# Kernel optimization log

Hardware: AMD Instinct MI355X
Metric: run time of the kernel (lower is better)

The kernel has to match this reference:

```python
import jax, jax.numpy as jnp
import numpy as np

B, N, D = 16, 128, 3          # batch, atoms per graph, spatial dims
C, L = 128, 3                 # hidden channels, EGNN layers
NUM_ATOM_TYPE, NUM_AA_TYPE = 54, 20
NUM_AA_MAX, NUM_VALID_SEQ = 30, 26   # num_aa_min=5 -> 30-5+1=26
ENC = NUM_ATOM_TYPE + NUM_AA_MAX + NUM_AA_TYPE + NUM_VALID_SEQ + 1  # 131


def setup_inputs() -> dict:
    key = jax.random.key(0)
    ks = jax.random.split(key, 16)
    f32 = jnp.float32
    def lin(k, fi, fo, scale=1.0):
        return (jax.random.normal(k, (L, fi, fo), f32) * (scale / np.sqrt(fi))).astype(f32)
    return {
        "t": jax.random.uniform(ks[0], (B, 1), f32),
        "x": jax.random.normal(ks[1], (B, N * D), f32),
        "atom_type": jax.random.randint(ks[2], (B, N), 0, NUM_ATOM_TYPE),
        "aa_pos": jax.random.randint(ks[3], (B, N), 0, NUM_AA_MAX),
        "aa_type": jax.random.randint(ks[4], (B, N), 0, NUM_AA_TYPE),
        "seq_len": jax.random.randint(ks[5], (B, 1), 5, 31),
        "node_mask": jnp.ones((B, N), f32),
        "emb_W": (jax.random.normal(ks[6], (ENC, C), f32) / np.sqrt(ENC)).astype(f32),
        "emb_b": jnp.zeros((C,), f32),
        "We1": lin(ks[7], 2 * C + 2, C), "be1": jnp.zeros((L, C), f32),
        "We2": lin(ks[8], C, C),        "be2": jnp.zeros((L, C), f32),
        "Wa": lin(ks[9], C, 1),         "ba": jnp.zeros((L, 1), f32),
        "Wn1": lin(ks[10], 2 * C, C),   "bn1": jnp.zeros((L, C), f32),
        "Wn2": lin(ks[11], C, C),       "bn2": jnp.zeros((L, C), f32),
        "Wc1": lin(ks[12], C, C),       "bc1": jnp.zeros((L, C), f32),
        "Wc2": lin(ks[13], C, 1, scale=0.01),
    }


def _forward(t, x, atom_type, aa_pos, aa_type, seq_len, node_mask,
             emb_W, emb_b, We1, be1, We2, be2, Wa, ba,
             Wn1, bn1, Wn2, bn2, Wc1, bc1, Wc2):
    mask = node_mask.reshape(B * N, 1)
    xf = x.reshape(B * N, D) * mask                       # masked coords

    # time feature: (B,1) -> (B*N,1)
    tt = jnp.repeat(t, N, axis=1).reshape(B * N, 1) * mask

    # one-hot node features (clamp(enc-1, min=0) then one_hot)
    oh_atom = jax.nn.one_hot(jnp.clip(atom_type - 1, 0), NUM_ATOM_TYPE)
    oh_pos = jax.nn.one_hot(jnp.clip(aa_pos - 1, 0), NUM_AA_MAX)
    oh_aa = jax.nn.one_hot(jnp.clip(aa_type - 1, 0), NUM_AA_TYPE)
    se = jnp.clip(seq_len - NUM_AA_MAX + NUM_VALID_SEQ - 1, 0)  # (B,1)
    oh_sl = jax.nn.one_hot(jnp.broadcast_to(se, (B, N)), NUM_VALID_SEQ)
    h = jnp.concatenate([oh_atom, oh_pos, oh_aa, oh_sl], axis=-1)
    h = h.reshape(B * N, -1) * mask
    h = jnp.concatenate([h, tt], axis=-1)                 # (B*N, ENC)

    # fully-connected edges (incl. self-edges, masked out by edge_mask)
    ii = jnp.arange(N)
    base = jnp.arange(B)[:, None, None] * N
    row = jnp.broadcast_to(base + ii[None, :, None], (B, N, N)).reshape(-1)
    col = jnp.broadcast_to(base + ii[None, None, :], (B, N, N)).reshape(-1)
    edge_mask = (node_mask[:, :, None] * node_mask[:, None, :]
                 * (1.0 - jnp.eye(N, dtype=node_mask.dtype))).reshape(-1, 1)

    edge_attr = jnp.sum((xf[row] - xf[col]) ** 2, axis=-1, keepdims=True)

    h = h @ emb_W + emb_b
    xcur = xf
    for l in range(L):
        diff = xcur[row] - xcur[col]                      # (E, 3)
        radial = jnp.sum(diff * diff, axis=-1, keepdims=True)
        m = jnp.concatenate([h[row], h[col], radial, edge_attr], axis=-1)
        m = jax.nn.silu(m @ We1[l] + be1[l])
        m = jax.nn.silu(m @ We2[l] + be2[l])
        m = m * jax.nn.sigmoid(m @ Wa[l] + ba[l])         # attention gate
        m = m * edge_mask
        # equivariant coordinate update
        c = jax.nn.silu(m @ Wc1[l] + bc1[l])
        trans = diff * jnp.tanh(c @ Wc2[l])
        xcur = (xcur + jax.ops.segment_sum(trans, row, num_segments=B * N)) * mask
        # node update (recurrent/residual)
        agg = jax.ops.segment_sum(m, row, num_segments=B * N)
        hn = jax.nn.silu(jnp.concatenate([h, agg], axis=-1) @ Wn1[l] + bn1[l])
        hn = hn @ Wn2[l] + bn2[l]
        h = (h + hn) * mask

    vel = ((xcur - xf) * mask).reshape(B, N, D)
    m3 = node_mask.reshape(B, N, 1)
    cnt = jnp.sum(m3, axis=1, keepdims=True)
    vel = vel - (jnp.sum(vel, axis=1, keepdims=True) / cnt) * m3
    return vel.reshape(B, N * D)


def reference(t, x, atom_type, aa_pos, aa_type, seq_len, node_mask,
              emb_W, emb_b, We1, be1, We2, be2, Wa, ba,
              Wn1, bn1, Wn2, bn2, Wc1, bc1, Wc2):
    return _forward(t, x, atom_type, aa_pos, aa_type, seq_len, node_mask,
                    emb_W, emb_b, We1, be1, We2, be2, Wa, ba,
                    Wn1, bn1, Wn2, bn2, Wc1, bc1, Wc2)
```

## Files before the change

kernel.cpp:

```cpp
#include <hip/hip_runtime.h>
#include <math.h>

#define CC 128

typedef float  f32x4  __attribute__((ext_vector_type(4)));
typedef short  s16x8  __attribute__((ext_vector_type(8)));
typedef __bf16 bf16x8 __attribute__((ext_vector_type(8)));

__device__ __forceinline__ float fsilu(float x) { return x / (1.0f + __expf(-x)); }
__device__ __forceinline__ float fsigm(float x) { return 1.0f / (1.0f + __expf(-x)); }
__device__ __forceinline__ float ftanh_(float x) { return 1.0f - 2.0f / (__expf(2.0f * x) + 1.0f); }

__device__ __forceinline__ void bsplit(float x, short& hi, short& lo) {
    unsigned xu = __float_as_uint(x);
    unsigned hr = (xu + 0x7FFFu + ((xu >> 16) & 1u)) & 0xFFFF0000u;
    float hf = __uint_as_float(hr);
    float r = x - hf;
    unsigned ru = __float_as_uint(r);
    unsigned lr = ru + 0x7FFFu + ((ru >> 16) & 1u);
    hi = (short)(hr >> 16);
    lo = (short)(lr >> 16);
}

__device__ __forceinline__ f32x4 mfma16(s16x8 a, s16x8 b, f32x4 c) {
    return __builtin_amdgcn_mfma_f32_16x16x32_bf16(
        __builtin_bit_cast(bf16x8, a), __builtin_bit_cast(bf16x8, b), c, 0, 0, 0);
}

__global__ __launch_bounds__(128) void egnn_init(
    const float* __restrict__ t, const float* __restrict__ x,
    const int* __restrict__ atomt, const int* __restrict__ aapos,
    const int* __restrict__ aatype, const int* __restrict__ slen,
    const float* __restrict__ nmask, const float* __restrict__ embW,
    const float* __restrict__ embB, float* __restrict__ h,
    float* __restrict__ xf, float* __restrict__ xA)
{
    const int n = blockIdx.x;
    const int c = threadIdx.x;
    const int b = n >> 7;
    const int i = n & 127;
    const float mi = nmask[n];
    int ia = atomt[n] - 1; if (ia < 0) ia = 0;
    int ip = aapos[n] - 1; if (ip < 0) ip = 0;
    int iq = aatype[n] - 1; if (iq < 0) iq = 0;
    int is = slen[b] - 5;  if (is < 0) is = 0;
    const float tt = t[b] * mi;
    float v = mi * (embW[ia * CC + c] + embW[(54 + ip) * CC + c] +
                    embW[(84 + iq) * CC + c] + embW[(104 + is) * CC + c]) +
              tt * embW[130 * CC + c] + embB[c];
    h[(size_t)n * CC + c] = v;
    if (c < 3) {
        float xv = x[b * 384 + i * 3 + c] * mi;
        xf[3 * n + c] = xv;
        xA[3 * n + c] = xv;
    }
}

__global__ __launch_bounds__(128) void egnn_wtprep(
    const float* __restrict__ We2, const float* __restrict__ Wc1,
    short* __restrict__ wt)
{
    const int blk = blockIdx.x;
    const int l = blk >> 5;
    const int mat = (blk >> 4) & 1;
    const int chunk = blk & 15;
    const int k = threadIdx.x;
    const float* W = (mat == 0 ? We2 : Wc1) + (size_t)l * CC * CC;
    short* hi = wt + (size_t)(l * 2 + mat) * 32768;
    short* lo = hi + 16384;
#pragma unroll
    for (int nn = 0; nn < 8; ++nn) {
        const int n = chunk * 8 + nn;
        short h_, l_;
        bsplit(W[k * CC + n], h_, l_);
        hi[n * CC + k] = h_;
        lo[n * CC + k] = l_;
    }
}

__global__ __launch_bounds__(128) void egnn_pq(
    const float* __restrict__ h, const float* __restrict__ We1,
    const float* __restrict__ be1, float* __restrict__ P, float* __restrict__ Q)
{
    __shared__ float hs[2][CC];
    const int c = threadIdx.x;
    const int n0 = blockIdx.x * 2;
    hs[0][c] = h[(size_t)n0 * CC + c];
    hs[1][c] = h[(size_t)(n0 + 1) * CC + c];
    __syncthreads();
    const float bv = be1[c];
    float p0 = bv, p1 = bv, q0 = 0.f, q1 = 0.f;
#pragma unroll 4
    for (int k = 0; k < CC; ++k) {
        const float wr = We1[k * CC + c];
        const float wc = We1[(CC + k) * CC + c];
        p0 = fmaf(hs[0][k], wr, p0); p1 = fmaf(hs[1][k], wr, p1);
        q0 = fmaf(hs[0][k], wc, q0); q1 = fmaf(hs[1][k], wc, q1);
    }
    P[(size_t)n0 * CC + c] = p0; P[(size_t)(n0 + 1) * CC + c] = p1;
    Q[(size_t)n0 * CC + c] = q0; Q[(size_t)(n0 + 1) * CC + c] = q1;
}

__global__ __launch_bounds__(256, 2) void egnn_edge(
    const float* __restrict__ P, const float* __restrict__ Q,
    const float* __restrict__ xcur, const float* __restrict__ xf,
    const float* __restrict__ nmask, const float* __restrict__ We1t,
    const short* __restrict__ w1hiP, const short* __restrict__ w2hiP,
    const float* __restrict__ be2, const float* __restrict__ Wa,
    const float* __restrict__ ba, const float* __restrict__ bc1,
    const float* __restrict__ Wc2,
    float* __restrict__ xnext, float* __restrict__ agg)
{
    extern __shared__ char smraw[];
    short* mhi = (short*)smraw;
    short* mlo = mhi + 16384;
    float* fb    = (float*)(mlo + 16384);
    float* diffs = fb;
    float* rjs   = fb + 384;
    float* eas   = fb + 512;
    float* emks  = fb + 640;
    float* pis   = fb + 768;
    float* wrads = fb + 896;
    float* weas  = fb + 1024;
    float* wass  = fb + 1152;
    float* wc2s  = fb + 1280;
    float* be2s  = fb + 1408;
    float* bc1s  = fb + 1536;
    float* aggp  = fb + 1664;
    float* trp   = fb + 2176;

    const int tid = threadIdx.x;
    const int w  = tid >> 6;
    const int lane = tid & 63;
    const int g  = lane >> 4;
    const int lj = lane & 15;
    const int n = blockIdx.x;
    const int b = n >> 7;
    const int i = n & 127;
    const int nb = b << 7;
    const float mi = nmask[n];

    const short* w1lo = w1hiP + 16384;
    const short* w2lo = w2hiP + 16384;

    if (tid < 128) {
        const int j = tid;
        const float xi0 = xcur[3 * n], xi1 = xcur[3 * n + 1], xi2 = xcur[3 * n + 2];
        const float xj0 = xcur[3 * (nb + j)], xj1 = xcur[3 * (nb + j) + 1], xj2 = xcur[3 * (nb + j) + 2];
        const float d0 = xi0 - xj0, d1 = xi1 - xj1, d2 = xi2 - xj2;
        diffs[3 * j] = d0; diffs[3 * j + 1] = d1; diffs[3 * j + 2] = d2;
        rjs[j] = d0 * d0 + d1 * d1 + d2 * d2;
        const float f0 = xf[3 * n] - xf[3 * (nb + j)];
        const float f1 = xf[3 * n + 1] - xf[3 * (nb + j) + 1];
        const float f2 = xf[3 * n + 2] - xf[3 * (nb + j) + 2];
        eas[j] = f0 * f0 + f1 * f1 + f2 * f2;
        emks[j] = mi * nmask[nb + j] * ((j == i) ? 0.0f : 1.0f);
    } else {
        const int c = tid - 128;
        pis[c]   = P[(size_t)n * CC + c];
        wrads[c] = We1t[c];
        weas[c]  = We1t[CC + c];
        wass[c]  = Wa[c];
        wc2s[c]  = Wc2[c];
        be2s[c]  = be2[c];
        bc1s[c]  = bc1[c];
    }
    __syncthreads();

    s16x8 ahi[2][4], alo[2][4];
#pragma unroll
    for (int mt = 0; mt < 2; ++mt) {
        const int j = (w << 5) + (mt << 4) + lj;
        const float r  = rjs[j];
        const float ea = eas[j];
        const float* Qj = Q + (size_t)(nb + j) * CC;
#pragma unroll
        for (int kt = 0; kt < 4; ++kt) {
            const int c0 = (kt << 5) + (g << 3);
            const float4 q0 = *reinterpret_cast<const float4*>(Qj + c0);
            const float4 q1 = *reinterpret_cast<const float4*>(Qj + c0 + 4);
            const float4 p0 = *reinterpret_cast<const float4*>(pis + c0);
            const float4 p1 = *reinterpret_cast<const float4*>(pis + c0 + 4);
            const float4 r0 = *reinterpret_cast<const float4*>(wrads + c0);
            const float4 r1 = *reinterpret_cast<const float4*>(wrads + c0 + 4);
            const float4 e0 = *reinterpret_cast<const float4*>(weas + c0);
            const float4 e1 = *reinterpret_cast<const float4*>(weas + c0 + 4);
            float vv[8];
            vv[0] = fsilu(p0.x + q0.x + r * r0.x + ea * e0.x);
            vv[1] = fsilu(p0.y + q0.y + r * r0.y + ea * e0.y);
            vv[2] = fsilu(p0.z + q0.z + r * r0.z + ea * e0.z);
            vv[3] = fsilu(p0.w + q0.w + r * r0.w + ea * e0.w);
            vv[4] = fsilu(p1.x + q1.x + r * r1.x + ea * e1.x);
            vv[5] = fsilu(p1.y + q1.y + r * r1.y + ea * e1.y);
            vv[6] = fsilu(p1.z + q1.z + r * r1.z + ea * e1.z);
            vv[7] = fsilu(p1.w + q1.w + r * r1.w + ea * e1.w);
#pragma unroll
            for (int e = 0; e < 8; ++e) {
                short h_, l_;
                bsplit(vv[e], h_, l_);
                ahi[mt][kt][e] = h_;
                alo[mt][kt][e] = l_;
            }
        }
    }

    f32x4 acc[2][8];
#pragma unroll
    for (int mt = 0; mt < 2; ++mt)
#pragma unroll
        for (int nt = 0; nt < 8; ++nt) acc[mt][nt] = (f32x4){0.f, 0.f, 0.f, 0.f};
#pragma unroll
    for (int kt = 0; kt < 4; ++kt) {
#pragma unroll
        for (int nt = 0; nt < 8; ++nt) {
            const int wo = ((nt << 4) + lj) * CC + (kt << 5) + (g << 3);
            const s16x8 bh = *reinterpret_cast<const s16x8*>(w1hiP + wo);
            const s16x8 bl = *reinterpret_cast<const s16x8*>(w1lo + wo);
#pragma unroll
            for (int mt = 0; mt < 2; ++mt) {
                acc[mt][nt] = mfma16(ahi[mt][kt], bh, acc[mt][nt]);
                acc[mt][nt] = mfma16(ahi[mt][kt], bl, acc[mt][nt]);
                acc[mt][nt] = mfma16(alo[mt][kt], bh, acc[mt][nt]);
            }
        }
    }

    float pa[2][4];
#pragma unroll
    for (int mt = 0; mt < 2; ++mt)
#pragma unroll
        for (int r = 0; r < 4; ++r) pa[mt][r] = 0.f;
#pragma unroll
    for (int mt = 0; mt < 2; ++mt)
#pragma unroll
        for (int nt = 0; nt < 8; ++nt) {
            const int c = (nt << 4) + lj;
            const float be = be2s[c], wa = wass[c];
#pragma unroll
            for (int r = 0; r < 4; ++r) {
                const float v = fsilu(acc[mt][nt][r] + be);
                acc[mt][nt][r] = v;
                pa[mt][r] = fmaf(v, wa, pa[mt][r]);
            }
        }
#pragma unroll
    for (int o = 1; o < 16; o <<= 1)
#pragma unroll
        for (int mt = 0; mt < 2; ++mt)
#pragma unroll
            for (int r = 0; r < 4; ++r) pa[mt][r] += __shfl_xor(pa[mt][r], o, 64);
    const float bav = ba[0];
    float gate[2][4];
#pragma unroll
    for (int mt = 0; mt < 2; ++mt)
#pragma unroll
        for (int r = 0; r < 4; ++r) {
            const int j = (w << 5) + (mt << 4) + (g << 2) + r;
            gate[mt][r] = fsigm(pa[mt][r] + bav) * emks[j];
        }
    float ap[8];
#pragma unroll
    for (int nt = 0; nt < 8; ++nt) ap[nt] = 0.f;
#pragma unroll
    for (int mt = 0; mt < 2; ++mt)
#pragma unroll
        for (int nt = 0; nt < 8; ++nt) {
            const int c = (nt << 4) + lj;
#pragma unroll
            for (int r = 0; r < 4; ++r) {
                const float mval = acc[mt][nt][r] * gate[mt][r];
                ap[nt] += mval;
                short h_, l_;
                bsplit(mval, h_, l_);
                const int j = (w << 5) + (mt << 4) + (g << 2) + r;
                const int idx = j * CC + (c ^ ((j & 7) << 3));
                mhi[idx] = h_;
                mlo[idx] = l_;
            }
        }
#pragma unroll
    for (int o = 16; o < 64; o <<= 1)
#pragma unroll
        for (int nt = 0; nt < 8; ++nt) ap[nt] += __shfl_xor(ap[nt], o, 64);
    if (g == 0) {
#pragma unroll
        for (int nt = 0; nt < 8; ++nt) aggp[(w << 7) + (nt << 4) + lj] = ap[nt];
    }
    __syncthreads();

    if (tid < 128) {
        agg[(size_t)n * CC + tid] =
            aggp[tid] + aggp[128 + tid] + aggp[256 + tid] + aggp[384 + tid];
    }

    s16x8 a2h[2][4], a2l[2][4];
#pragma unroll
    for (int mt = 0; mt < 2; ++mt) {
        const int j = (w << 5) + (mt << 4) + lj;
#pragma unroll
        for (int kt = 0; kt < 4; ++kt) {
            const int ofs = j * CC + ((((kt << 5) + (g << 3))) ^ ((j & 7) << 3));
            a2h[mt][kt] = *reinterpret_cast<const s16x8*>(mhi + ofs);
            a2l[mt][kt] = *reinterpret_cast<const s16x8*>(mlo + ofs);
        }
    }
    f32x4 acc2[2][8];
#pragma unroll
    for (int mt = 0; mt < 2; ++mt)
#pragma unroll
        for (int nt = 0; nt < 8; ++nt) acc2[mt][nt] = (f32x4){0.f, 0.f, 0.f, 0.f};
#pragma unroll
    for (int kt = 0; kt < 4; ++kt) {
#pragma unroll
        for (int nt = 0; nt < 8; ++nt) {
            const int wo = ((nt << 4) + lj) * CC + (kt << 5) + (g << 3);
            const s16x8 bh = *reinterpret_cast<const s16x8*>(w2hiP + wo);
            const s16x8 bl = *reinterpret_cast<const s16x8*>(w2lo + wo);
#pragma unroll
            for (int mt = 0; mt < 2; ++mt) {
                acc2[mt][nt] = mfma16(a2h[mt][kt], bh, acc2[mt][nt]);
                acc2[mt][nt] = mfma16(a2h[mt][kt], bl, acc2[mt][nt]);
                acc2[mt][nt] = mfma16(a2l[mt][kt], bh, acc2[mt][nt]);
            }
        }
    }

    float dt[2][4];
#pragma unroll
    for (int mt = 0; mt < 2; ++mt)
#pragma unroll
        for (int r = 0; r < 4; ++r) dt[mt][r] = 0.f;
#pragma unroll
    for (int mt = 0; mt < 2; ++mt)
#pragma unroll
        for (int nt = 0; nt < 8; ++nt) {
            const int c = (nt << 4) + lj;
            const float bc = bc1s[c], wc = wc2s[c];
#pragma unroll
            for (int r = 0; r < 4; ++r)
                dt[mt][r] = fmaf(fsilu(acc2[mt][nt][r] + bc), wc, dt[mt][r]);
        }
#pragma unroll
    for (int o = 1; o < 16; o <<= 1)
#pragma unroll
        for (int mt = 0; mt < 2; ++mt)
#pragma unroll
            for (int r = 0; r < 4; ++r) dt[mt][r] += __shfl_xor(dt[mt][r], o, 64);
    if (lj == 0) {
        float t0 = 0.f, t1 = 0.f, t2 = 0.f;
#pragma unroll
        for (int mt = 0; mt < 2; ++mt)
#pragma unroll
            for (int r = 0; r < 4; ++r) {
                const int j = (w << 5) + (mt << 4) + (g << 2) + r;
                const float ts = ftanh_(dt[mt][r]);
                t0 = fmaf(diffs[3 * j    ], ts, t0);
                t1 = fmaf(diffs[3 * j + 1], ts, t1);
                t2 = fmaf(diffs[3 * j + 2], ts, t2);
            }
        const int slot = (w << 2) + g;
        trp[slot * 4 + 0] = t0; trp[slot * 4 + 1] = t1; trp[slot * 4 + 2] = t2;
    }
    __syncthreads();
    if (tid < 3) {
        float s = 0.f;
#pragma unroll
        for (int q = 0; q < 16; ++q) s += trp[q * 4 + tid];
        xnext[3 * n + tid] = (xcur[3 * n + tid] + s) * mi;
    }
}

__global__ __launch_bounds__(128) void egnn_node(
    float* __restrict__ h, const float* __restrict__ agg,
    const float* __restrict__ nmask,
    const float* __restrict__ Wn1, const float* __restrict__ bn1,
    const float* __restrict__ Wn2, const float* __restrict__ bn2)
{
    __shared__ float hs[2][CC], as_[2][CC], hn[2][CC];
    const int c = threadIdx.x;
    const int n0 = blockIdx.x * 2;
    hs[0][c] = h[(size_t)n0 * CC + c];
    hs[1][c] = h[(size_t)(n0 + 1) * CC + c];
    as_[0][c] = agg[(size_t)n0 * CC + c];
    as_[1][c] = agg[(size_t)(n0 + 1) * CC + c];
    __syncthreads();
    float a0 = bn1[c], a1 = a0;
#pragma unroll 4
    for (int k = 0; k < CC; ++k) {
        const float wv = Wn1[k * CC + c];
        a0 = fmaf(hs[0][k], wv, a0); a1 = fmaf(hs[1][k], wv, a1);
    }
#pragma unroll 4
    for (int k = 0; k < CC; ++k) {
        const float wv = Wn1[(CC + k) * CC + c];
        a0 = fmaf(as_[0][k], wv, a0); a1 = fmaf(as_[1][k], wv, a1);
    }
    hn[0][c] = fsilu(a0); hn[1][c] = fsilu(a1);
    __syncthreads();
    a0 = bn2[c]; a1 = a0;
#pragma unroll 4
    for (int k = 0; k < CC; ++k) {
        const float wv = Wn2[k * CC + c];
        a0 = fmaf(hn[0][k], wv, a0); a1 = fmaf(hn[1][k], wv, a1);
    }
    h[(size_t)n0 * CC + c]       = (hs[0][c] + a0) * nmask[n0];
    h[(size_t)(n0 + 1) * CC + c] = (hs[1][c] + a1) * nmask[n0 + 1];
}

__global__ __launch_bounds__(128) void egnn_final(
    const float* __restrict__ xcur, const float* __restrict__ xf,
    const float* __restrict__ nmask, float* __restrict__ out)
{
    __shared__ float red[128][4];
    const int i = threadIdx.x, b = blockIdx.x;
    const int n = b * 128 + i;
    const float mi = nmask[n];
    const float v0 = (xcur[3 * n    ] - xf[3 * n    ]) * mi;
    const float v1 = (xcur[3 * n + 1] - xf[3 * n + 1]) * mi;
    const float v2 = (xcur[3 * n + 2] - xf[3 * n + 2]) * mi;
    red[i][0] = v0; red[i][1] = v1; red[i][2] = v2; red[i][3] = mi;
    __syncthreads();
    for (int s = 64; s > 0; s >>= 1) {
        if (i < s) {
            red[i][0] += red[i + s][0]; red[i][1] += red[i + s][1];
            red[i][2] += red[i + s][2]; red[i][3] += red[i + s][3];
        }
        __syncthreads();
    }
    const float inv = 1.0f / red[0][3];
    out[b * 384 + i * 3 + 0] = v0 - red[0][0] * inv * mi;
    out[b * 384 + i * 3 + 1] = v1 - red[0][1] * inv * mi;
    out[b * 384 + i * 3 + 2] = v2 - red[0][2] * inv * mi;
}

extern "C" void kernel_launch(void* const* d_in, const int* in_sizes, int n_in,
                              void* d_out, int out_size, void* d_ws, size_t ws_size,
                              hipStream_t stream) {
    const float* t     = (const float*)d_in[0];
    const float* x     = (const float*)d_in[1];
    const int*   atomt = (const int*)d_in[2];
    const int*   aapos = (const int*)d_in[3];
    const int*   aatyp = (const int*)d_in[4];
    const int*   slen  = (const int*)d_in[5];
    const float* nmask = (const float*)d_in[6];
    const float* embW  = (const float*)d_in[7];
    const float* embB  = (const float*)d_in[8];
    const float* We1   = (const float*)d_in[9];
    const float* be1   = (const float*)d_in[10];
    const float* We2   = (const float*)d_in[11];
    const float* be2   = (const float*)d_in[12];
    const float* Wa    = (const float*)d_in[13];
    const float* ba    = (const float*)d_in[14];
    const float* Wn1   = (const float*)d_in[15];
    const float* bn1   = (const float*)d_in[16];
    const float* Wn2   = (const float*)d_in[17];
    const float* bn2   = (const float*)d_in[18];
    const float* Wc1   = (const float*)d_in[19];
    const float* bc1   = (const float*)d_in[20];
    const float* Wc2   = (const float*)d_in[21];

    float* ws  = (float*)d_ws;
    float* h   = ws;
    float* P   = ws + 262144;
    float* Q   = ws + 524288;
    float* agg = ws + 786432;
    float* xA  = ws + 1048576;
    float* xB  = ws + 1054720;
    float* xf  = ws + 1060864;
    short* wt  = (short*)(ws + 1067008);
    float* out = (float*)d_out;

    egnn_init<<<2048, 128, 0, stream>>>(t, x, atomt, aapos, aatyp, slen, nmask,
                                        embW, embB, h, xf, xA);
    egnn_wtprep<<<96, 128, 0, stream>>>(We2, Wc1, wt);

    const size_t edge_lds = 65536 + 2240 * sizeof(float);
    float* xc = xA;
    float* xn = xB;
    for (int l = 0; l < 3; ++l) {
        egnn_pq<<<1024, 128, 0, stream>>>(h, We1 + (size_t)l * 258 * CC,
                                          be1 + l * CC, P, Q);
        egnn_edge<<<2048, 256, edge_lds, stream>>>(
            P, Q, xc, xf, nmask,
            We1 + (size_t)l * 258 * CC + 256 * CC,
            wt + (size_t)(l * 2 + 0) * 32768,
            wt + (size_t)(l * 2 + 1) * 32768,
            be2 + l * CC, Wa + l * CC, ba + l, bc1 + l * CC, Wc2 + l * CC,
            xn, agg);
        egnn_node<<<1024, 128, 0, stream>>>(h, agg, nmask,
                                            Wn1 + (size_t)l * 2 * CC * CC, bn1 + l * CC,
                                            Wn2 + (size_t)l * CC * CC, bn2 + l * CC);
        float* tmp = xc; xc = xn; xn = tmp;
    }
    egnn_final<<<16, 128, 0, stream>>>(xc, xf, nmask, out);
}
```

Measured before the change: 702.4 us.

## Halve edge-kernel LDS by reusing one message buffer and overlaying scratch

The edge kernel now stages the hi and lo bf16 halves of the gated message through a single shared buffer in two passes, and overlays the early per-edge scratch arrays with the later aggregation arrays. This cuts LDS per block roughly in half, and launch bounds rise to 4 blocks per CU to raise occupancy. It also skips the last layer's node update, whose output h is never used for the velocity. In exchange it adds a barrier plus extra LDS round trips, and the tighter register budget could cause spills.

```diff
diff --git a/kernel.cpp b/kernel.cpp
--- a/kernel.cpp
+++ b/kernel.cpp
@@ -101,7 +101,7 @@
     Q[(size_t)n0 * CC + c] = q0; Q[(size_t)(n0 + 1) * CC + c] = q1;
 }
 
-__global__ __launch_bounds__(256, 2) void egnn_edge(
+__global__ __launch_bounds__(256, 4) void egnn_edge(
     const float* __restrict__ P, const float* __restrict__ Q,
     const float* __restrict__ xcur, const float* __restrict__ xf,
     const float* __restrict__ nmask, const float* __restrict__ We1t,
@@ -112,22 +112,22 @@
     float* __restrict__ xnext, float* __restrict__ agg)
 {
     extern __shared__ char smraw[];
-    short* mhi = (short*)smraw;
-    short* mlo = mhi + 16384;
-    float* fb    = (float*)(mlo + 16384);
+    short* ms    = (short*)smraw;
+    float* fb    = (float*)(ms + 16384);
     float* diffs = fb;
-    float* rjs   = fb + 384;
-    float* eas   = fb + 512;
-    float* emks  = fb + 640;
-    float* pis   = fb + 768;
-    float* wrads = fb + 896;
-    float* weas  = fb + 1024;
-    float* wass  = fb + 1152;
-    float* wc2s  = fb + 1280;
-    float* be2s  = fb + 1408;
-    float* bc1s  = fb + 1536;
-    float* aggp  = fb + 1664;
-    float* trp   = fb + 2176;
+    float* emks  = fb + 384;
+    float* wass  = fb + 512;
+    float* wc2s  = fb + 640;
+    float* be2s  = fb + 768;
+    float* bc1s  = fb + 896;
+    float* ovl   = fb + 1024;
+    float* rjs   = ovl;
+    float* eas   = ovl + 128;
+    float* pis   = ovl + 256;
+    float* wrads = ovl + 384;
+    float* weas  = ovl + 512;
+    float* aggp  = ovl;
+    float* trp   = ovl + 512;
 
     const int tid = threadIdx.x;
     const int w  = tid >> 6;
@@ -203,6 +203,7 @@
             }
         }
     }
+    __syncthreads();
 
     f32x4 acc[2][8];
 #pragma unroll
@@ -258,11 +259,14 @@
             const int j = (w << 5) + (mt << 4) + (g << 2) + r;
             gate[mt][r] = fsigm(pa[mt][r] + bav) * emks[j];
         }
+
     float ap[8];
 #pragma unroll
     for (int nt = 0; nt < 8; ++nt) ap[nt] = 0.f;
-#pragma unroll
-    for (int mt = 0; mt < 2; ++mt)
+    s16x8 a2h[2][4], a2l[2][4];
+#pragma unroll
+    for (int mt = 0; mt < 2; ++mt) {
+        short llo[8][4];
 #pragma unroll
         for (int nt = 0; nt < 8; ++nt) {
             const int c = (nt << 4) + lj;
@@ -274,10 +278,31 @@
                 bsplit(mval, h_, l_);
                 const int j = (w << 5) + (mt << 4) + (g << 2) + r;
                 const int idx = j * CC + (c ^ ((j & 7) << 3));
-                mhi[idx] = h_;
-                mlo[idx] = l_;
-            }
-        }
+                ms[idx] = h_;
+                llo[nt][r] = l_;
+            }
+        }
+        const int jr = (w << 5) + (mt << 4) + lj;
+#pragma unroll
+        for (int kt = 0; kt < 4; ++kt) {
+            const int ofs = jr * CC + ((((kt << 5) + (g << 3))) ^ ((jr & 7) << 3));
+            a2h[mt][kt] = *reinterpret_cast<const s16x8*>(ms + ofs);
+        }
+#pragma unroll
+        for (int nt = 0; nt < 8; ++nt) {
+#pragma unroll
+            for (int r = 0; r < 4; ++r) {
+                const int j = (w << 5) + (mt << 4) + (g << 2) + r;
+                const int idx = j * CC + ((((nt << 4) + lj)) ^ ((j & 7) << 3));
+                ms[idx] = llo[nt][r];
+            }
+        }
+#pragma unroll
+        for (int kt = 0; kt < 4; ++kt) {
+            const int ofs = jr * CC + ((((kt << 5) + (g << 3))) ^ ((jr & 7) << 3));
+            a2l[mt][kt] = *reinterpret_cast<const s16x8*>(ms + ofs);
+        }
+    }
 #pragma unroll
     for (int o = 16; o < 64; o <<= 1)
 #pragma unroll
@@ -293,17 +318,6 @@
             aggp[tid] + aggp[128 + tid] + aggp[256 + tid] + aggp[384 + tid];
     }
 
-    s16x8 a2h[2][4], a2l[2][4];
-#pragma unroll
-    for (int mt = 0; mt < 2; ++mt) {
-        const int j = (w << 5) + (mt << 4) + lj;
-#pragma unroll
-        for (int kt = 0; kt < 4; ++kt) {
-            const int ofs = j * CC + ((((kt << 5) + (g << 3))) ^ ((j & 7) << 3));
-            a2h[mt][kt] = *reinterpret_cast<const s16x8*>(mhi + ofs);
-            a2l[mt][kt] = *reinterpret_cast<const s16x8*>(mlo + ofs);
-        }
-    }
     f32x4 acc2[2][8];
 #pragma unroll
     for (int mt = 0; mt < 2; ++mt)
@@ -474,7 +488,7 @@
                                         embW, embB, h, xf, xA);
     egnn_wtprep<<<96, 128, 0, stream>>>(We2, Wc1, wt);
 
-    const size_t edge_lds = 65536 + 2240 * sizeof(float);
+    const size_t edge_lds = 16384 * sizeof(short) + 1664 * sizeof(float);
     float* xc = xA;
     float* xn = xB;
     for (int l = 0; l < 3; ++l) {
@@ -487,9 +501,11 @@
             wt + (size_t)(l * 2 + 1) * 32768,
             be2 + l * CC, Wa + l * CC, ba + l, bc1 + l * CC, Wc2 + l * CC,
             xn, agg);
-        egnn_node<<<1024, 128, 0, stream>>>(h, agg, nmask,
-                                            Wn1 + (size_t)l * 2 * CC * CC, bn1 + l * CC,
-                                            Wn2 + (size_t)l * CC * CC, bn2 + l * CC);
+        if (l < 2) {
+            egnn_node<<<1024, 128, 0, stream>>>(h, agg, nmask,
+                                                Wn1 + (size_t)l * 2 * CC * CC, bn1 + l * CC,
+                                                Wn2 + (size_t)l * CC * CC, bn2 + l * CC);
+        }
         float* tmp = xc; xc = xn; xn = tmp;
     }
     egnn_final<<<16, 128, 0, stream>>>(xc, xf, nmask, out);
```

After: 836.6 us. 19.1% more time.
